# Performance work log

Hardware: AMD Instinct MI355X
Metric: run time of the kernel (lower is better)

## Reference

```python
import jax, jax.numpy as jnp
import numpy as np

B, N, D, H = 32, 8192, 128, 128


def setup_inputs() -> dict:
    key = jax.random.key(0)
    ks = jax.random.split(key, 9)
    s = lambda k, shp, fan: jax.random.normal(k, shp, jnp.float32) / np.sqrt(fan)
    return {
        "x": jax.random.normal(ks[0], (B, N, D), jnp.float32),
        "Wg1": s(ks[1], (D, H), D), "bg1": jnp.zeros((H,), jnp.float32),
        "Wg2": s(ks[2], (H, 1), H), "bg2": jnp.zeros((1,), jnp.float32),
        "Wn1": s(ks[3], (D, H), D), "bn1": jnp.zeros((H,), jnp.float32),
        "Wn2": s(ks[4], (H, H), H), "bn2": jnp.zeros((H,), jnp.float32),
    }


def reference(x, Wg1, bg1, Wg2, bg2, Wn1, bn1, Wn2, bn2):
    # gate_nn: Linear -> SiLU -> Linear(->1); scores per node
    gate = jnp.einsum("bnd,dh->bnh", x, Wg1) + bg1
    gate = jax.nn.silu(gate)
    gate = jnp.einsum("bnh,ho->bno", gate, Wg2) + bg2  # [B,N,1]
    # nn: Linear -> SiLU -> Linear; transformed node features
    h = jax.nn.silu(jnp.einsum("bnd,dh->bnh", x, Wn1) + bn1)
    h = jnp.einsum("bnh,hk->bnk", h, Wn2) + bn2  # [B,N,H]
    # segment softmax over nodes of each graph (segments == batch dim here)
    attn = jax.nn.softmax(gate, axis=1)  # [B,N,1]
    # weighted-sum pooling per graph
    return jnp.sum(attn * h, axis=1)  # [B,H]
```

## Files before the change

### kernel.cpp

```cpp
#include <hip/hip_runtime.h>

#define B_ 32
#define N_ 8192
#define D_ 128
#define H_ 128
#define R_ (B_ * N_)

#define NBLK 1024
#define TILES 4

typedef _Float16 f16;
typedef __attribute__((ext_vector_type(4))) _Float16 f16x4;
typedef __attribute__((ext_vector_type(8))) _Float16 f16x8;
typedef __attribute__((ext_vector_type(4))) float f32x4;

static constexpr size_t WPACK_OFF = 0;
static constexpr size_t VPART_OFF = 98304;
static constexpr size_t SPART_OFF = VPART_OFF + (size_t)NBLK * 128 * 4;

__device__ __forceinline__ float silu_f(float v) {
    return v * __builtin_amdgcn_rcpf(1.0f + __expf(-v));
}

__device__ __forceinline__ f32x4 mfma16(f16x8 a, f16x8 b, f32x4 c) {
    return __builtin_amdgcn_mfma_f32_16x16x32_f16(a, b, c, 0, 0, 0);
}

__global__ void k0_prepack(const float* __restrict__ Wg1,
                           const float* __restrict__ Wn1,
                           const float* __restrict__ Wn2,
                           f16* __restrict__ wp) {
    int tid = blockIdx.x * 256 + threadIdx.x;
    int m    = tid >> 14;
    int r    = tid & 16383;
    int j    = r & 7;
    int lane = (r >> 3) & 63;
    int kc   = (r >> 9) & 3;
    int nt   = r >> 11;
    int k = kc * 32 + (lane >> 4) * 8 + j;
    int n = nt * 16 + (lane & 15);
    const float* W = (m == 0) ? Wg1 : (m == 1) ? Wn1 : Wn2;
    wp[tid] = (f16)W[k * 128 + n];
}

__global__ __launch_bounds__(512) void k1_fused(
        const float* __restrict__ x,
        const float* __restrict__ bg1, const float* __restrict__ wg2,
        const float* __restrict__ bg2, const float* __restrict__ bn1,
        const f16* __restrict__ wp,
        float* __restrict__ vpart, float* __restrict__ spart) {
    __shared__ f16 xlds[64 * 128];
    __shared__ f16 h1lds[64 * 128];
    __shared__ float gpart[8][64];

    const int tid  = threadIdx.x;
    const int w    = tid >> 6;
    const int lane = tid & 63;
    const int q    = lane >> 4;
    const int c    = lane & 15;

    const f16x8* wpv = (const f16x8*)wp;
    f16x8 fg1[4], fn1[4], fn2[4];
#pragma unroll
    for (int kc = 0; kc < 4; ++kc) {
        int base = (w * 4 + kc) * 64 + lane;
        fg1[kc] = wpv[base];
        fn1[kc] = wpv[2048 + base];
        fn2[kc] = wpv[4096 + base];
    }
    float bg1q[4], wg2q[4], bn1q[4];
#pragma unroll
    for (int r = 0; r < 4; ++r) {
        int col = w * 16 + q * 4 + r;
        bg1q[r] = bg1[col];
        wg2q[r] = wg2[col];
        bn1q[r] = bn1[col];
    }
    const float bg2v = bg2[0];

    const int loh_e = (q * 16 + (c ^ q)) * 8;
    const int loh_o = (q * 16 + (c ^ (q | 4))) * 8;
    const int kc2 = w >> 1;
    const int q2  = (w & 1) * 2 + (q >> 1);
    const int v2  = ((kc2 & 1) << 2) | q2;
    const int h1w_base = kc2 * 512 + (q2 * 16 + (c ^ v2)) * 8 + (q & 1) * 4;

    f16* sdst[4];
#pragma unroll
    for (int s = 0; s < 4; ++s) {
        int e   = s * 512 + tid;
        int row = e >> 5, c4 = e & 31;
        int mt = row >> 4, cc = row & 15;
        int kc = c4 >> 3, qq = (c4 >> 1) & 3, j = (c4 & 1) * 4;
        int sw = (c4 >> 1) & 7;
        sdst[s] = &xlds[((mt * 4 + kc) * 64 + qq * 16 + (cc ^ sw)) * 8 + j];
    }

    float V[4] = {0.f, 0.f, 0.f, 0.f};
    float Sl = 0.f;

    const long rowbase = (long)blockIdx.x * (TILES * 64);
    const float4* xg = (const float4*)x + rowbase * 32;

    float4 pre[4];
#pragma unroll
    for (int s = 0; s < 4; ++s) pre[s] = xg[s * 512 + tid];

    for (int t = 0; t < TILES; ++t) {
#pragma unroll
        for (int s = 0; s < 4; ++s) {
            float4 vv = pre[s];
            f16x4 hv = {(f16)vv.x, (f16)vv.y, (f16)vv.z, (f16)vv.w};
            *(f16x4*)sdst[s] = hv;
        }
        __syncthreads();

        if (t < TILES - 1) {
            const float4* xn = xg + (t + 1) * 2048;
#pragma unroll
            for (int s = 0; s < 4; ++s) pre[s] = xn[s * 512 + tid];
        }

#pragma unroll
        for (int mt = 0; mt < 4; ++mt) {
            f16x8 a[4];
#pragma unroll
            for (int kc = 0; kc < 4; ++kc)
                a[kc] = *(const f16x8*)&xlds[(mt * 4 + kc) * 512 +
                                             ((kc & 1) ? loh_o : loh_e)];
            f32x4 ag = {0.f, 0.f, 0.f, 0.f};
            f32x4 an = {0.f, 0.f, 0.f, 0.f};
#pragma unroll
            for (int kc = 0; kc < 4; ++kc) {
                ag = mfma16(fg1[kc], a[kc], ag);
                an = mfma16(fn1[kc], a[kc], an);
            }
            f16x4 h4;
#pragma unroll
            for (int r = 0; r < 4; ++r) h4[r] = (f16)silu_f(an[r] + bn1q[r]);
            *(f16x4*)&h1lds[mt * 2048 + h1w_base] = h4;
            float p = 0.f;
#pragma unroll
            for (int r = 0; r < 4; ++r)
                p += silu_f(ag[r] + bg1q[r]) * wg2q[r];
            p += __shfl_xor(p, 16);
            p += __shfl_xor(p, 32);
            if (lane < 16) gpart[w][mt * 16 + lane] = p;
        }
        __syncthreads();

        float e[4];
#pragma unroll
        for (int mt = 0; mt < 4; ++mt) {
            float g = bg2v;
#pragma unroll
            for (int w2 = 0; w2 < 8; ++w2) g += gpart[w2][mt * 16 + c];
            e[mt] = __expf(g);
        }
        if (w == 0 && q == 0) {
#pragma unroll
            for (int mt = 0; mt < 4; ++mt) Sl += e[mt];
        }

#pragma unroll
        for (int mt = 0; mt < 4; ++mt) {
            f16x8 b[4];
#pragma unroll
            for (int kc = 0; kc < 4; ++kc)
                b[kc] = *(const f16x8*)&h1lds[(mt * 4 + kc) * 512 +
                                              ((kc & 1) ? loh_o : loh_e)];
            f32x4 acc = {0.f, 0.f, 0.f, 0.f};
#pragma unroll
            for (int kc = 0; kc < 4; ++kc)
                acc = mfma16(fn2[kc], b[kc], acc);
#pragma unroll
            for (int r = 0; r < 4; ++r) V[r] += e[mt] * acc[r];
        }
    }

#pragma unroll
    for (int m = 1; m < 16; m <<= 1) {
#pragma unroll
        for (int r = 0; r < 4; ++r) V[r] += __shfl_xor(V[r], m);
    }
    if ((lane & 15) == 0) {
        float4 o = {V[0], V[1], V[2], V[3]};
        *(float4*)&vpart[(long)blockIdx.x * 128 + w * 16 + q * 4] = o;
    }
    if (w == 0) {
#pragma unroll
        for (int m = 1; m < 16; m <<= 1) Sl += __shfl_xor(Sl, m);
        if (lane == 0) spart[blockIdx.x] = Sl;
    }
}

__global__ void k2_combine(const float* __restrict__ vpart,
                           const float* __restrict__ spart,
                           const float* __restrict__ bn2,
                           float* __restrict__ out) {
    const int b = blockIdx.x;
    const int j = threadIdx.x;
    const int P = NBLK / B_;
    float v = 0.f, s = 0.f;
#pragma unroll
    for (int k = 0; k < P; ++k) {
        v += vpart[(long)(b * P + k) * 128 + j];
        s += spart[b * P + k];
    }
    out[b * 128 + j] = v / s + bn2[j];
}

extern "C" void kernel_launch(void* const* d_in, const int* in_sizes, int n_in,
                              void* d_out, int out_size, void* d_ws, size_t ws_size,
                              hipStream_t stream) {
    const float* x   = (const float*)d_in[0];
    const float* Wg1 = (const float*)d_in[1];
    const float* bg1 = (const float*)d_in[2];
    const float* Wg2 = (const float*)d_in[3];
    const float* bg2 = (const float*)d_in[4];
    const float* Wn1 = (const float*)d_in[5];
    const float* bn1 = (const float*)d_in[6];
    const float* Wn2 = (const float*)d_in[7];
    const float* bn2 = (const float*)d_in[8];
    float* out = (float*)d_out;

    char* ws = (char*)d_ws;
    f16*   wp    = (f16*)(ws + WPACK_OFF);
    float* vpart = (float*)(ws + VPART_OFF);
    float* spart = (float*)(ws + SPART_OFF);

    k0_prepack<<<192, 256, 0, stream>>>(Wg1, Wn1, Wn2, wp);
    k1_fused<<<NBLK, 512, 0, stream>>>(x, bg1, Wg2, bg2, bn1, wp, vpart, spart);
    k2_combine<<<32, 128, 0, stream>>>(vpart, spart, bn2, out);
}
```

Measured before the change: 221.2 us.

## Split fused kernel into one-tile blocks of 256 threads, two column groups per wave

The fused MLP-pooling kernel now runs 4096 blocks of 256 threads, each processing a single 64-row tile, instead of 1024 blocks of 512 threads looping over four tiles with register prefetch. Each wave holds weight fragments for two 16-column groups, so the MFMA work per wave doubles and the gate partial reduction shrinks to four waves. The combine kernel is widened to 256 threads to reduce 128 partials per graph. The aim is more blocks in flight to hide memory latency. The cost is losing the in-block prefetch pipeline and reloading the packed weights four times as often, which adds L2 traffic.

```diff
diff --git a/kernel.cpp b/kernel.cpp
--- a/kernel.cpp
+++ b/kernel.cpp
@@ -6,8 +6,7 @@
 #define H_ 128
 #define R_ (B_ * N_)
 
-#define NBLK 1024
-#define TILES 4
+#define NBLK 4096
 
 typedef _Float16 f16;
 typedef __attribute__((ext_vector_type(4))) _Float16 f16x4;
@@ -43,7 +42,7 @@
     wp[tid] = (f16)W[k * 128 + n];
 }
 
-__global__ __launch_bounds__(512) void k1_fused(
+__global__ __launch_bounds__(256, 2) void k1_fused(
         const float* __restrict__ x,
         const float* __restrict__ bg1, const float* __restrict__ wg2,
         const float* __restrict__ bg2, const float* __restrict__ bn1,
@@ -51,7 +50,7 @@
         float* __restrict__ vpart, float* __restrict__ spart) {
     __shared__ f16 xlds[64 * 128];
     __shared__ f16 h1lds[64 * 128];
-    __shared__ float gpart[8][64];
+    __shared__ float gpart[4][64];
 
     const int tid  = threadIdx.x;
     const int w    = tid >> 6;
@@ -59,135 +58,137 @@
     const int q    = lane >> 4;
     const int c    = lane & 15;
 
+    const long rowbase = (long)blockIdx.x * 64;
+    const float4* xg = (const float4*)x + rowbase * 32;
+    float4 xv[8];
+#pragma unroll
+    for (int s = 0; s < 8; ++s) xv[s] = xg[s * 256 + tid];
+
     const f16x8* wpv = (const f16x8*)wp;
-    f16x8 fg1[4], fn1[4], fn2[4];
-#pragma unroll
-    for (int kc = 0; kc < 4; ++kc) {
-        int base = (w * 4 + kc) * 64 + lane;
-        fg1[kc] = wpv[base];
-        fn1[kc] = wpv[2048 + base];
-        fn2[kc] = wpv[4096 + base];
-    }
-    float bg1q[4], wg2q[4], bn1q[4];
-#pragma unroll
-    for (int r = 0; r < 4; ++r) {
-        int col = w * 16 + q * 4 + r;
-        bg1q[r] = bg1[col];
-        wg2q[r] = wg2[col];
-        bn1q[r] = bn1[col];
-    }
+    f16x8 fg1[2][4], fn1[2][4], fn2[2][4];
+#pragma unroll
+    for (int s = 0; s < 2; ++s)
+#pragma unroll
+        for (int kc = 0; kc < 4; ++kc) {
+            int base = ((2 * w + s) * 4 + kc) * 64 + lane;
+            fg1[s][kc] = wpv[base];
+            fn1[s][kc] = wpv[2048 + base];
+            fn2[s][kc] = wpv[4096 + base];
+        }
+    float bg1q[2][4], wg2q[2][4], bn1q[2][4];
+#pragma unroll
+    for (int s = 0; s < 2; ++s)
+#pragma unroll
+        for (int r = 0; r < 4; ++r) {
+            int col = (2 * w + s) * 16 + q * 4 + r;
+            bg1q[s][r] = bg1[col];
+            wg2q[s][r] = wg2[col];
+            bn1q[s][r] = bn1[col];
+        }
     const float bg2v = bg2[0];
 
     const int loh_e = (q * 16 + (c ^ q)) * 8;
     const int loh_o = (q * 16 + (c ^ (q | 4))) * 8;
-    const int kc2 = w >> 1;
-    const int q2  = (w & 1) * 2 + (q >> 1);
-    const int v2  = ((kc2 & 1) << 2) | q2;
-    const int h1w_base = kc2 * 512 + (q2 * 16 + (c ^ v2)) * 8 + (q & 1) * 4;
-
-    f16* sdst[4];
-#pragma unroll
-    for (int s = 0; s < 4; ++s) {
-        int e   = s * 512 + tid;
+    int h1wb[2];
+#pragma unroll
+    for (int s = 0; s < 2; ++s) {
+        int q2 = s * 2 + (q >> 1);
+        int v2 = ((w & 1) << 2) | q2;
+        h1wb[s] = w * 512 + (q2 * 16 + (c ^ v2)) * 8 + (q & 1) * 4;
+    }
+
+#pragma unroll
+    for (int s = 0; s < 8; ++s) {
+        int e   = s * 256 + tid;
         int row = e >> 5, c4 = e & 31;
         int mt = row >> 4, cc = row & 15;
         int kc = c4 >> 3, qq = (c4 >> 1) & 3, j = (c4 & 1) * 4;
         int sw = (c4 >> 1) & 7;
-        sdst[s] = &xlds[((mt * 4 + kc) * 64 + qq * 16 + (cc ^ sw)) * 8 + j];
-    }
-
-    float V[4] = {0.f, 0.f, 0.f, 0.f};
-    float Sl = 0.f;
-
-    const long rowbase = (long)blockIdx.x * (TILES * 64);
-    const float4* xg = (const float4*)x + rowbase * 32;
-
-    float4 pre[4];
-#pragma unroll
-    for (int s = 0; s < 4; ++s) pre[s] = xg[s * 512 + tid];
-
-    for (int t = 0; t < TILES; ++t) {
-#pragma unroll
-        for (int s = 0; s < 4; ++s) {
-            float4 vv = pre[s];
-            f16x4 hv = {(f16)vv.x, (f16)vv.y, (f16)vv.z, (f16)vv.w};
-            *(f16x4*)sdst[s] = hv;
-        }
-        __syncthreads();
-
-        if (t < TILES - 1) {
-            const float4* xn = xg + (t + 1) * 2048;
-#pragma unroll
-            for (int s = 0; s < 4; ++s) pre[s] = xn[s * 512 + tid];
-        }
-
-#pragma unroll
-        for (int mt = 0; mt < 4; ++mt) {
-            f16x8 a[4];
-#pragma unroll
-            for (int kc = 0; kc < 4; ++kc)
-                a[kc] = *(const f16x8*)&xlds[(mt * 4 + kc) * 512 +
-                                             ((kc & 1) ? loh_o : loh_e)];
-            f32x4 ag = {0.f, 0.f, 0.f, 0.f};
-            f32x4 an = {0.f, 0.f, 0.f, 0.f};
-#pragma unroll
-            for (int kc = 0; kc < 4; ++kc) {
-                ag = mfma16(fg1[kc], a[kc], ag);
-                an = mfma16(fn1[kc], a[kc], an);
+        float4 vv = xv[s];
+        f16x4 hv = {(f16)vv.x, (f16)vv.y, (f16)vv.z, (f16)vv.w};
+        *(f16x4*)&xlds[((mt * 4 + kc) * 64 + qq * 16 + (cc ^ sw)) * 8 + j] = hv;
+    }
+    __syncthreads();
+
+#pragma unroll
+    for (int mt = 0; mt < 4; ++mt) {
+        f16x8 a[4];
+#pragma unroll
+        for (int kc = 0; kc < 4; ++kc)
+            a[kc] = *(const f16x8*)&xlds[(mt * 4 + kc) * 512 +
+                                         ((kc & 1) ? loh_o : loh_e)];
+        f32x4 ag[2] = {{0.f,0.f,0.f,0.f},{0.f,0.f,0.f,0.f}};
+        f32x4 an[2] = {{0.f,0.f,0.f,0.f},{0.f,0.f,0.f,0.f}};
+#pragma unroll
+        for (int kc = 0; kc < 4; ++kc) {
+#pragma unroll
+            for (int s = 0; s < 2; ++s) {
+                ag[s] = mfma16(fg1[s][kc], a[kc], ag[s]);
+                an[s] = mfma16(fn1[s][kc], a[kc], an[s]);
             }
+        }
+#pragma unroll
+        for (int s = 0; s < 2; ++s) {
             f16x4 h4;
 #pragma unroll
-            for (int r = 0; r < 4; ++r) h4[r] = (f16)silu_f(an[r] + bn1q[r]);
-            *(f16x4*)&h1lds[mt * 2048 + h1w_base] = h4;
-            float p = 0.f;
+            for (int r = 0; r < 4; ++r) h4[r] = (f16)silu_f(an[s][r] + bn1q[s][r]);
+            *(f16x4*)&h1lds[mt * 2048 + h1wb[s]] = h4;
+        }
+        float p = 0.f;
+#pragma unroll
+        for (int s = 0; s < 2; ++s)
 #pragma unroll
             for (int r = 0; r < 4; ++r)
-                p += silu_f(ag[r] + bg1q[r]) * wg2q[r];
-            p += __shfl_xor(p, 16);
-            p += __shfl_xor(p, 32);
-            if (lane < 16) gpart[w][mt * 16 + lane] = p;
-        }
-        __syncthreads();
-
-        float e[4];
-#pragma unroll
-        for (int mt = 0; mt < 4; ++mt) {
-            float g = bg2v;
-#pragma unroll
-            for (int w2 = 0; w2 < 8; ++w2) g += gpart[w2][mt * 16 + c];
-            e[mt] = __expf(g);
-        }
-        if (w == 0 && q == 0) {
-#pragma unroll
-            for (int mt = 0; mt < 4; ++mt) Sl += e[mt];
-        }
-
-#pragma unroll
-        for (int mt = 0; mt < 4; ++mt) {
-            f16x8 b[4];
-#pragma unroll
-            for (int kc = 0; kc < 4; ++kc)
-                b[kc] = *(const f16x8*)&h1lds[(mt * 4 + kc) * 512 +
-                                              ((kc & 1) ? loh_o : loh_e)];
-            f32x4 acc = {0.f, 0.f, 0.f, 0.f};
-#pragma unroll
-            for (int kc = 0; kc < 4; ++kc)
-                acc = mfma16(fn2[kc], b[kc], acc);
-#pragma unroll
-            for (int r = 0; r < 4; ++r) V[r] += e[mt] * acc[r];
-        }
-    }
-
-#pragma unroll
-    for (int m = 1; m < 16; m <<= 1) {
-#pragma unroll
-        for (int r = 0; r < 4; ++r) V[r] += __shfl_xor(V[r], m);
-    }
-    if ((lane & 15) == 0) {
-        float4 o = {V[0], V[1], V[2], V[3]};
-        *(float4*)&vpart[(long)blockIdx.x * 128 + w * 16 + q * 4] = o;
+                p += silu_f(ag[s][r] + bg1q[s][r]) * wg2q[s][r];
+        p += __shfl_xor(p, 16);
+        p += __shfl_xor(p, 32);
+        if (lane < 16) gpart[w][mt * 16 + lane] = p;
+    }
+    __syncthreads();
+
+    float e4[4];
+#pragma unroll
+    for (int mt = 0; mt < 4; ++mt) {
+        float g = bg2v + gpart[0][mt * 16 + c] + gpart[1][mt * 16 + c]
+                       + gpart[2][mt * 16 + c] + gpart[3][mt * 16 + c];
+        e4[mt] = __expf(g);
+    }
+
+    float V[2][4] = {{0.f,0.f,0.f,0.f},{0.f,0.f,0.f,0.f}};
+#pragma unroll
+    for (int mt = 0; mt < 4; ++mt) {
+        f16x8 b[4];
+#pragma unroll
+        for (int kc = 0; kc < 4; ++kc)
+            b[kc] = *(const f16x8*)&h1lds[(mt * 4 + kc) * 512 +
+                                          ((kc & 1) ? loh_o : loh_e)];
+        f32x4 acc[2] = {{0.f,0.f,0.f,0.f},{0.f,0.f,0.f,0.f}};
+#pragma unroll
+        for (int kc = 0; kc < 4; ++kc)
+#pragma unroll
+            for (int s = 0; s < 2; ++s)
+                acc[s] = mfma16(fn2[s][kc], b[kc], acc[s]);
+#pragma unroll
+        for (int s = 0; s < 2; ++s)
+#pragma unroll
+            for (int r = 0; r < 4; ++r) V[s][r] += e4[mt] * acc[s][r];
+    }
+
+#pragma unroll
+    for (int m = 1; m < 16; m <<= 1)
+#pragma unroll
+        for (int s = 0; s < 2; ++s)
+#pragma unroll
+            for (int r = 0; r < 4; ++r) V[s][r] += __shfl_xor(V[s][r], m);
+    if (c == 0) {
+#pragma unroll
+        for (int s = 0; s < 2; ++s) {
+            float4 o = {V[s][0], V[s][1], V[s][2], V[s][3]};
+            *(float4*)&vpart[(long)blockIdx.x * 128 + (2 * w + s) * 16 + q * 4] = o;
+        }
     }
     if (w == 0) {
+        float Sl = e4[0] + e4[1] + e4[2] + e4[3];
 #pragma unroll
         for (int m = 1; m < 16; m <<= 1) Sl += __shfl_xor(Sl, m);
         if (lane == 0) spart[blockIdx.x] = Sl;
@@ -199,15 +200,31 @@
                            const float* __restrict__ bn2,
                            float* __restrict__ out) {
     const int b = blockIdx.x;
-    const int j = threadIdx.x;
-    const int P = NBLK / B_;
-    float v = 0.f, s = 0.f;
-#pragma unroll
-    for (int k = 0; k < P; ++k) {
-        v += vpart[(long)(b * P + k) * 128 + j];
-        s += spart[b * P + k];
-    }
-    out[b * 128 + j] = v / s + bn2[j];
+    const int t = threadIdx.x;
+    const int j = t & 127;
+    const int half = t >> 7;
+
+    const float* vp = vpart + (long)b * 128 * 128;
+    float v = 0.f;
+#pragma unroll
+    for (int k = 0; k < 64; ++k)
+        v += vp[(half * 64 + k) * 128 + j];
+
+    __shared__ float vred[128];
+    __shared__ float sred[4];
+    if (half == 0) vred[j] = v;
+
+    float s = (t < 128) ? spart[b * 128 + t] : 0.f;
+#pragma unroll
+    for (int m = 1; m < 64; m <<= 1) s += __shfl_xor(s, m);
+    if (t < 128 && (t & 63) == 0) sred[t >> 6] = s;
+    __syncthreads();
+    if (half == 1) vred[j] += v;
+    __syncthreads();
+    if (t < 128) {
+        float denom = sred[0] + sred[1];
+        out[b * 128 + t] = vred[t] / denom + bn2[t];
+    }
 }
 
 extern "C" void kernel_launch(void* const* d_in, const int* in_sizes, int n_in,
@@ -230,6 +247,6 @@
     float* spart = (float*)(ws + SPART_OFF);
 
     k0_prepack<<<192, 256, 0, stream>>>(Wg1, Wn1, Wn2, wp);
-    k1_fused<<<NBLK, 512, 0, stream>>>(x, bg1, Wg2, bg2, bn1, wp, vpart, spart);
-    k2_combine<<<32, 128, 0, stream>>>(vpart, spart, bn2, out);
-}
+    k1_fused<<<NBLK, 256, 0, stream>>>(x, bg1, Wg2, bg2, bn1, wp, vpart, spart);
+    k2_combine<<<32, 256, 0, stream>>>(vpart, spart, bn2, out);
+}
```

Result: faster. 212.1 us (-4.1%).
